# Performance work log

Hardware: AMD Instinct MI355X
Metric: run time of the kernel (lower is better)

The kernel has to match this reference:

```python
import jax, jax.numpy as jnp
import numpy as np

COMMITMENT = 0.25

def setup_inputs() -> dict:
    key = jax.random.key(0)
    k1, k2 = jax.random.split(key)
    x = jax.random.normal(k1, (64, 256, 32, 32), dtype=jnp.float32)
    embed = jax.random.normal(k2, (256, 1024), dtype=jnp.float32)  # [emb_dim, num_emb]
    return {"x": x, "embed": embed}

def reference(x, embed):
    # x: [B, C, H, W] -> NHWC
    xt = jnp.transpose(x, (0, 2, 3, 1))              # [B, H, W, C]
    B, H, W, C = xt.shape
    flat = xt.reshape(-1, C)                         # [N, C]
    # squared euclidean distances to each codebook column
    dist = (jnp.sum(flat * flat, axis=1, keepdims=True)
            - 2.0 * flat @ embed
            + jnp.sum(embed * embed, axis=0, keepdims=True))  # [N, num_emb]
    embed_idx = jnp.argmin(dist, axis=1).reshape(B, H, W)     # [B, H, W]
    quantize = embed.T[embed_idx]                    # [B, H, W, C]
    e_latent_loss = jnp.mean((jax.lax.stop_gradient(quantize) - xt) ** 2)
    q_latent_loss = jnp.mean((quantize - jax.lax.stop_gradient(xt)) ** 2)
    loss = q_latent_loss + COMMITMENT * e_latent_loss
    # straight-through estimator
    quantize = xt + jax.lax.stop_gradient(quantize - xt)
    quantize = jnp.transpose(quantize, (0, 3, 1, 2))  # back to NCHW
    return quantize, loss, embed_idx
```

## Files before the change

### kernel.cpp

```cpp
#include <hip/hip_runtime.h>

#define CDIM 256
#define HW   1024
#define NPIX 65536
#define KDIM 1024
#define TAU  0.5f
#define RB   4
#define SWZ(c) (((c) & 31) ^ (((c) >> 3) & 24))

using bf16x8 = __attribute__((ext_vector_type(8))) short;
using f32x4  = __attribute__((ext_vector_type(4))) float;
typedef unsigned int u32;

static __device__ __forceinline__ unsigned short f2bf(float v) {
    union { float f; unsigned u; } a; a.f = v;
    unsigned u = a.u;
    u += 0x7fffu + ((u >> 16) & 1u);
    return (unsigned short)(u >> 16);
}

static __device__ __forceinline__ void gload_lds16(const void* g, void* s) {
    __builtin_amdgcn_global_load_lds(
        (const __attribute__((address_space(1))) u32*)g,
        (__attribute__((address_space(3))) u32*)s,
        16, 0, 0);
}

__global__ void ee_kernel(const float* __restrict__ embed, float* __restrict__ ee) {
    int k = blockIdx.x * 256 + threadIdx.x;
    float s = 0.f;
#pragma unroll 8
    for (int c = 0; c < CDIM; ++c) {
        float v = embed[c * KDIM + k];
        s += v * v;
    }
    ee[k] = s;
}

__global__ void transpose_e(const float* __restrict__ embed, float* __restrict__ embedT) {
    __shared__ float tl[32][33];
    const int t = threadIdx.x;
    const int j = t & 31, r = t >> 5;
    const int k0 = (blockIdx.x & 31) * 32;
    const int c0 = (blockIdx.x >> 5) * 32;
#pragma unroll
    for (int rr = 0; rr < 4; ++rr) {
        int c = r * 4 + rr;
        tl[c][j] = embed[(size_t)(c0 + c) * KDIM + k0 + j];
    }
    __syncthreads();
#pragma unroll
    for (int rr = 0; rr < 4; ++rr) {
        int k = r * 4 + rr;
        embedT[(size_t)(k0 + k) * CDIM + c0 + j] = tl[j][k];
    }
}

__global__ void prep_e(const float* __restrict__ embed, short* __restrict__ e_hi) {
    int tid = blockIdx.x * 256 + threadIdx.x;
    int l  = tid & 63;
    int f  = tid >> 6;
    int nf = f & 3;
    int ks = (f >> 2) & 7;
    int nh = (f >> 5) & 1;
    int nt = f >> 6;
    int n  = nt * 128 + (nh * 4 + nf) * 16 + (l & 15);
    int c0 = ks * 32 + (l >> 4) * 8;
    bf16x8 h8;
#pragma unroll
    for (int j = 0; j < 8; ++j)
        h8[j] = (short)f2bf(-2.0f * embed[(c0 + j) * KDIM + n]);
    *(bf16x8*)&e_hi[(size_t)tid * 8] = h8;
}

__launch_bounds__(256, 2)
__global__ void vq_gemm(const float* __restrict__ x, const short* __restrict__ e_hi,
                        const float* __restrict__ ee,
                        float* __restrict__ hv1, float* __restrict__ hv2,
                        int* __restrict__ hidx) {
    __shared__ short Bs[2][8192];
    const int t  = threadIdx.x;
    const int l  = t & 63;
    const int w  = t >> 6;
    const int lr = l & 15;
    const int lg = l >> 4;
    const int tile    = blockIdx.x >> 2;
    const int quarter = blockIdx.x & 3;
    const int px0 = tile * 256 + w * 64;
    const int b   = px0 >> 10;
    const int p0  = px0 & 1023;
    const float* xb = x + (size_t)b * CDIM * HW;

    const int c_first = quarter * 8;
    {
        const int slab = w * 4;
        const char* srcb = (const char*)e_hi +
            (size_t)(((c_first >> 2) * 2 + ((c_first >> 1) & 1)) * 32 + (c_first & 1) * 2) * 1024 + l * 16;
        char* dstb = (char*)&Bs[0][0] + (size_t)slab * 1024 + l * 16;
#pragma unroll
        for (int i = 0; i < 4; ++i) {
            int s = slab + i;
            gload_lds16(srcb + (size_t)((s >> 1) * 4 + (s & 1)) * 1024, dstb + (size_t)i * 1024);
        }
    }

    bf16x8 a[4][8];
#pragma unroll
    for (int mf = 0; mf < 4; ++mf) {
#pragma unroll
        for (int ks = 0; ks < 8; ++ks) {
            const float* p = xb + (size_t)(ks * 32 + lg * 8) * HW + p0 + mf * 16 + lr;
            float v[8];
#pragma unroll
            for (int j = 0; j < 8; ++j) v[j] = p[(size_t)j * HW];
#pragma unroll
            for (int j = 0; j < 8; ++j) a[mf][ks][j] = (short)f2bf(v[j]);
        }
    }

    float minv[16], min2v[16];
    int   mini[16];
#pragma unroll
    for (int r = 0; r < 16; ++r) { minv[r] = 3.4e38f; min2v[r] = 3.4e38f; mini[r] = 0; }

    __syncthreads();

    for (int cc = 0; cc < 8; ++cc) {
        const int c   = c_first + cc;
        const int cur = cc & 1;
        if (cc < 7) {
            const int cn = c + 1;
            const int slab = w * 4;
            const char* srcb = (const char*)e_hi +
                (size_t)(((cn >> 2) * 2 + ((cn >> 1) & 1)) * 32 + (cn & 1) * 2) * 1024 + l * 16;
            char* dstb = (char*)&Bs[cur ^ 1][0] + (size_t)slab * 1024 + l * 16;
#pragma unroll
            for (int i = 0; i < 4; ++i) {
                int s = slab + i;
                gload_lds16(srcb + (size_t)((s >> 1) * 4 + (s & 1)) * 1024, dstb + (size_t)i * 1024);
            }
        }

        f32x4 acc[4][2];
#pragma unroll
        for (int mf = 0; mf < 4; ++mf)
#pragma unroll
            for (int nfi = 0; nfi < 2; ++nfi)
                acc[mf][nfi] = (f32x4){0.f, 0.f, 0.f, 0.f};

#pragma unroll
        for (int ks = 0; ks < 8; ++ks) {
#pragma unroll
            for (int nfi = 0; nfi < 2; ++nfi) {
                bf16x8 bh = *(const bf16x8*)&Bs[cur][((ks * 2 + nfi) * 64 + l) * 8];
#pragma unroll
                for (int mf = 0; mf < 4; ++mf)
                    acc[mf][nfi] = __builtin_amdgcn_mfma_f32_16x16x32_bf16(a[mf][ks], bh, acc[mf][nfi], 0, 0, 0);
            }
        }

#pragma unroll
        for (int nfi = 0; nfi < 2; ++nfi) {
            const int kg = c * 32 + nfi * 16 + lr;
            const float eev = ee[kg];
#pragma unroll
            for (int mf = 0; mf < 4; ++mf)
#pragma unroll
                for (int j = 0; j < 4; ++j) {
                    const int r = mf * 4 + j;
                    float m = acc[mf][nfi][j] + eev;
                    bool lt = m < minv[r];
                    float sec = lt ? minv[r] : m;
                    minv[r] = lt ? m : minv[r];
                    mini[r] = lt ? kg : mini[r];
                    min2v[r] = fminf(min2v[r], sec);
                }
        }
        __syncthreads();
    }

#pragma unroll
    for (int r = 0; r < 16; ++r) {
        float v1 = minv[r]; int i1 = mini[r]; float v2 = min2v[r];
#pragma unroll
        for (int mask = 1; mask < 16; mask <<= 1) {
            float ov1 = __shfl_xor(v1, mask, 64);
            int   oi1 = __shfl_xor(i1, mask, 64);
            float ov2 = __shfl_xor(v2, mask, 64);
            float vmax = fmaxf(v1, ov1);
            v2 = fminf(fminf(v2, ov2), vmax);
            bool take = (ov1 < v1) || (ov1 == v1 && oi1 < i1);
            v1 = take ? ov1 : v1;
            i1 = take ? oi1 : i1;
        }
        if (lr == 0) {
            int px = px0 + (r >> 2) * 16 + lg * 4 + (r & 3);
            int o = quarter * NPIX + px;
            hv1[o] = v1; hv2[o] = v2; hidx[o] = i1;
        }
    }
}

__global__ void merge_quarters(const float* __restrict__ hv1, const float* __restrict__ hv2,
                               const int* __restrict__ hidx, int* __restrict__ idx_out,
                               int* __restrict__ worklist, int* __restrict__ wcount) {
    int px = blockIdx.x * 256 + threadIdx.x;
    float v1 = hv1[px], v2 = hv2[px];
    int   i1 = hidx[px];
#pragma unroll
    for (int q = 1; q < 4; ++q) {
        float va = hv1[q * NPIX + px];
        float sa = hv2[q * NPIX + px];
        int   ia = hidx[q * NPIX + px];
        if (va < v1) {
            v2 = fminf(v1, sa);
            v1 = va; i1 = ia;
        } else {
            v2 = fminf(v2, va);
        }
    }
    idx_out[px] = i1;
    if (v2 - v1 < TAU) {
        int pos = atomicAdd(wcount, 1);
        worklist[pos] = px;
    }
}

__launch_bounds__(256)
__global__ void vq_rescue(const float* __restrict__ x, const float* __restrict__ embed,
                          const float* __restrict__ ee,
                          const int* __restrict__ worklist, const int* __restrict__ wcount,
                          int* __restrict__ idx_out) {
    __shared__ float xs[RB][CDIM];
    __shared__ int   pxs[RB];
    __shared__ float redv[4][RB];
    __shared__ int   redi[4][RB];
    const int t  = threadIdx.x;
    const int wv = t >> 6, ln = t & 63;
    const int cnt = *wcount;
    for (int base = blockIdx.x * RB; base < cnt; base += gridDim.x * RB) {
        const int nb = min(RB, cnt - base);
        __syncthreads();
        if (t < RB) pxs[t] = worklist[base + (t < nb ? t : nb - 1)];
        __syncthreads();
#pragma unroll
        for (int i = 0; i < RB; ++i) {
            int gn = pxs[i];
            xs[i][t] = x[(size_t)(gn >> 10) * CDIM * HW + (size_t)t * HW + (gn & 1023)];
        }
        __syncthreads();

        float4 acc[RB];
#pragma unroll
        for (int i = 0; i < RB; ++i) acc[i] = make_float4(0.f, 0.f, 0.f, 0.f);
#pragma unroll 4
        for (int c = 0; c < CDIM; ++c) {
            float4 ev = *(const float4*)&embed[c * KDIM + t * 4];
#pragma unroll
            for (int i = 0; i < RB; ++i) {
                float xv = xs[i][c];
                acc[i].x = fmaf(xv, ev.x, acc[i].x);
                acc[i].y = fmaf(xv, ev.y, acc[i].y);
                acc[i].z = fmaf(xv, ev.z, acc[i].z);
                acc[i].w = fmaf(xv, ev.w, acc[i].w);
            }
        }
        const float4 eev = *(const float4*)&ee[t * 4];
#pragma unroll
        for (int i = 0; i < RB; ++i) {
            float d0 = fmaf(-2.f, acc[i].x, eev.x);
            float d1 = fmaf(-2.f, acc[i].y, eev.y);
            float d2 = fmaf(-2.f, acc[i].z, eev.z);
            float d3 = fmaf(-2.f, acc[i].w, eev.w);
            float v = d0; int ix = t * 4;
            if (d1 < v) { v = d1; ix = t * 4 + 1; }
            if (d2 < v) { v = d2; ix = t * 4 + 2; }
            if (d3 < v) { v = d3; ix = t * 4 + 3; }
#pragma unroll
            for (int mask = 1; mask < 64; mask <<= 1) {
                float ov = __shfl_xor(v, mask, 64);
                int   oi = __shfl_xor(ix, mask, 64);
                bool take = (ov < v) || (ov == v && oi < ix);
                v = take ? ov : v; ix = take ? oi : ix;
            }
            if (ln == 0) { redv[wv][i] = v; redi[wv][i] = ix; }
        }
        __syncthreads();
        if (t < nb) {
            float fv = redv[0][t]; int fi = redi[0][t];
#pragma unroll
            for (int q = 1; q < 4; ++q) {
                float v = redv[q][t]; int ix = redi[q][t];
                if (v < fv || (v == fv && ix < fi)) { fv = v; fi = ix; }
            }
            idx_out[pxs[t]] = fi;
        }
    }
}

__launch_bounds__(256)
__global__ void vq_epilogue(const float* __restrict__ x, const float* __restrict__ embed,
                            const float* __restrict__ embedT, int useT,
                            const int* __restrict__ idx_in, float* __restrict__ out_q,
                            float* __restrict__ out_idx, float* __restrict__ partials) {
    __shared__ float q[16384];
    __shared__ int   idxs[128];
    __shared__ float lred[4];
    const int t = threadIdx.x;
    const int w = t >> 6, l = t & 63;
    const int n0 = blockIdx.x * 128;
    const int b  = n0 >> 10;

    if (t < 128) idxs[t] = idx_in[n0 + t];
    __syncthreads();
    if (t < 128) out_idx[n0 + t] = (float)idxs[t];

    const int j  = t >> 2;
    const int qd = t & 3;
    float lsum = 0.f;

#pragma unroll
    for (int pass = 0; pass < 2; ++pass) {
        const int myidx = idxs[pass * 64 + j];
        if (useT) {
            const float4* src4 = (const float4*)embedT + (size_t)myidx * 64;
#pragma unroll
            for (int i = 0; i < 16; ++i) {
                float4 v = src4[qd * 16 + i];
                int c = qd * 64 + i * 4;
                q[(c + 0) * 64 + (j ^ SWZ(c + 0))] = v.x;
                q[(c + 1) * 64 + (j ^ SWZ(c + 1))] = v.y;
                q[(c + 2) * 64 + (j ^ SWZ(c + 2))] = v.z;
                q[(c + 3) * 64 + (j ^ SWZ(c + 3))] = v.w;
            }
        } else {
#pragma unroll 4
            for (int i = 0; i < 64; ++i) {
                int c = qd * 64 + i;
                q[c * 64 + (j ^ SWZ(c))] = embed[(size_t)c * KDIM + myidx];
            }
        }
        __syncthreads();

        const int p0 = (n0 & 1023) + pass * 64;
        const size_t xbase = (size_t)b * CDIM * HW + p0;
#pragma unroll 8
        for (int ci = 0; ci < 64; ++ci) {
            int c = w * 64 + ci;
            float qv = q[c * 64 + (l ^ SWZ(c))];
            float xv = x[xbase + (size_t)c * HW + l];
            out_q[xbase + (size_t)c * HW + l] = qv;
            float d = qv - xv;
            lsum = fmaf(d, d, lsum);
        }
        __syncthreads();
    }

#pragma unroll
    for (int off = 32; off > 0; off >>= 1)
        lsum += __shfl_down(lsum, off, 64);
    if (l == 0) lred[w] = lsum;
    __syncthreads();
    if (t == 0)
        partials[blockIdx.x] = (lred[0] + lred[1]) + (lred[2] + lred[3]);
}

__global__ void loss_kernel(const float* __restrict__ partials, float* __restrict__ out_loss) {
    __shared__ float s[256];
    s[threadIdx.x] = partials[threadIdx.x] + partials[threadIdx.x + 256];
    __syncthreads();
    for (int off = 128; off > 0; off >>= 1) {
        if (threadIdx.x < off) s[threadIdx.x] += s[threadIdx.x + off];
        __syncthreads();
    }
    if (threadIdx.x == 0)
        out_loss[0] = 1.25f * s[0] / 16777216.0f;
}

extern "C" void kernel_launch(void* const* d_in, const int* in_sizes, int n_in,
                              void* d_out, int out_size, void* d_ws, size_t ws_size,
                              hipStream_t stream) {
    const float* x     = (const float*)d_in[0];
    const float* embed = (const float*)d_in[1];
    float* out_q    = (float*)d_out;
    float* out_loss = out_q + (size_t)NPIX * CDIM;
    float* out_idx  = out_loss + 1;
    int*   idx_i32  = (int*)out_idx;

    short* e_hi     = (short*)out_q;
    int*   worklist = (int*)(out_q + 131072);
    float* hv1      = out_q + 196608;
    float* hv2      = out_q + 458752;
    int*   hidx     = (int*)(out_q + 720896);

    float* ws       = (float*)d_ws;
    float* ee       = ws;
    int*   wcount   = (int*)(ws + 1024);
    float* partials = ws + 1088;
    float* embedT   = ws + 1600;
    int useT = (ws_size >= (size_t)(1600 + 262144) * sizeof(float)) ? 1 : 0;

    ee_kernel<<<KDIM / 256, 256, 0, stream>>>(embed, ee);
    if (useT) transpose_e<<<256, 256, 0, stream>>>(embed, embedT);
    prep_e<<<128, 256, 0, stream>>>(embed, e_hi);
    hipMemsetAsync(wcount, 0, 4, stream);
    vq_gemm<<<1024, 256, 0, stream>>>(x, e_hi, ee, hv1, hv2, hidx);
    merge_quarters<<<NPIX / 256, 256, 0, stream>>>(hv1, hv2, hidx, idx_i32, worklist, wcount);
    vq_rescue<<<1024, 256, 0, stream>>>(x, embed, ee, worklist, wcount, idx_i32);
    vq_epilogue<<<NPIX / 128, 256, 0, stream>>>(x, embed, useT ? embedT : embed, useT,
                                                idx_i32, out_q, out_idx, partials);
    loss_kernel<<<1, 256, 0, stream>>>(partials, out_loss);
}
```

Before: 189.9 us.

## Pack distance and index into sortable keys, halve GEMM tile for higher occupancy

The vq_gemm kernel now processes 32 pixels per wave instead of 64 and launches twice as many blocks, with launch bounds raised to 4 blocks per CU, to cut register pressure. The running min/second-min tracking is replaced by packed uint32 keys: distances are biased by +2048 so they stay positive, their low 10 mantissa bits are replaced with the codebook index, and plain integer min/max does the argmin. This drops the separate index registers and makes the shuffle reduction cheaper. The truncated distances lose precision, so the rescue threshold TAU is raised to 1.0, which may send more pixels to the exact rescue path.

```diff
diff --git a/kernel.cpp b/kernel.cpp
--- a/kernel.cpp
+++ b/kernel.cpp
@@ -4,7 +4,7 @@
 #define HW   1024
 #define NPIX 65536
 #define KDIM 1024
-#define TAU  0.5f
+#define TAU  1.0f
 #define RB   4
 #define SWZ(c) (((c) & 31) ^ (((c) >> 3) & 24))
 
@@ -26,7 +26,15 @@
         16, 0, 0);
 }
 
-__global__ void ee_kernel(const float* __restrict__ embed, float* __restrict__ ee) {
+static __device__ __forceinline__ u32 fbits(float f) {
+    union { float f; u32 u; } a; a.f = f; return a.u;
+}
+static __device__ __forceinline__ float bitsf(u32 u) {
+    union { u32 u; float f; } a; a.u = u; return a.f;
+}
+
+__global__ void ee_kernel(const float* __restrict__ embed, float* __restrict__ ee,
+                          float* __restrict__ eeb) {
     int k = blockIdx.x * 256 + threadIdx.x;
     float s = 0.f;
 #pragma unroll 8
@@ -35,6 +43,7 @@
         s += v * v;
     }
     ee[k] = s;
+    eeb[k] = s + 2048.0f;
 }
 
 __global__ void transpose_e(const float* __restrict__ embed, float* __restrict__ embedT) {
@@ -73,9 +82,9 @@
     *(bf16x8*)&e_hi[(size_t)tid * 8] = h8;
 }
 
-__launch_bounds__(256, 2)
+__launch_bounds__(256, 4)
 __global__ void vq_gemm(const float* __restrict__ x, const short* __restrict__ e_hi,
-                        const float* __restrict__ ee,
+                        const float* __restrict__ eeb,
                         float* __restrict__ hv1, float* __restrict__ hv2,
                         int* __restrict__ hidx) {
     __shared__ short Bs[2][8192];
@@ -84,9 +93,9 @@
     const int w  = t >> 6;
     const int lr = l & 15;
     const int lg = l >> 4;
-    const int tile    = blockIdx.x >> 2;
-    const int quarter = blockIdx.x & 3;
-    const int px0 = tile * 256 + w * 64;
+    const int tile    = blockIdx.x & 511;
+    const int quarter = blockIdx.x >> 9;
+    const int px0 = tile * 128 + w * 32;
     const int b   = px0 >> 10;
     const int p0  = px0 & 1023;
     const float* xb = x + (size_t)b * CDIM * HW;
@@ -104,9 +113,9 @@
         }
     }
 
-    bf16x8 a[4][8];
-#pragma unroll
-    for (int mf = 0; mf < 4; ++mf) {
+    bf16x8 a[2][8];
+#pragma unroll
+    for (int mf = 0; mf < 2; ++mf) {
 #pragma unroll
         for (int ks = 0; ks < 8; ++ks) {
             const float* p = xb + (size_t)(ks * 32 + lg * 8) * HW + p0 + mf * 16 + lr;
@@ -118,10 +127,9 @@
         }
     }
 
-    float minv[16], min2v[16];
-    int   mini[16];
-#pragma unroll
-    for (int r = 0; r < 16; ++r) { minv[r] = 3.4e38f; min2v[r] = 3.4e38f; mini[r] = 0; }
+    u32 min1k[8], min2k[8];
+#pragma unroll
+    for (int r = 0; r < 8; ++r) { min1k[r] = 0xFFFFFFFFu; min2k[r] = 0xFFFFFFFFu; }
 
     __syncthreads();
 
@@ -141,9 +149,9 @@
             }
         }
 
-        f32x4 acc[4][2];
-#pragma unroll
-        for (int mf = 0; mf < 4; ++mf)
+        f32x4 acc[2][2];
+#pragma unroll
+        for (int mf = 0; mf < 2; ++mf)
 #pragma unroll
             for (int nfi = 0; nfi < 2; ++nfi)
                 acc[mf][nfi] = (f32x4){0.f, 0.f, 0.f, 0.f};
@@ -154,7 +162,7 @@
             for (int nfi = 0; nfi < 2; ++nfi) {
                 bf16x8 bh = *(const bf16x8*)&Bs[cur][((ks * 2 + nfi) * 64 + l) * 8];
 #pragma unroll
-                for (int mf = 0; mf < 4; ++mf)
+                for (int mf = 0; mf < 2; ++mf)
                     acc[mf][nfi] = __builtin_amdgcn_mfma_f32_16x16x32_bf16(a[mf][ks], bh, acc[mf][nfi], 0, 0, 0);
             }
         }
@@ -162,41 +170,36 @@
 #pragma unroll
         for (int nfi = 0; nfi < 2; ++nfi) {
             const int kg = c * 32 + nfi * 16 + lr;
-            const float eev = ee[kg];
-#pragma unroll
-            for (int mf = 0; mf < 4; ++mf)
+            const float ebv = eeb[kg];
+#pragma unroll
+            for (int mf = 0; mf < 2; ++mf)
 #pragma unroll
                 for (int j = 0; j < 4; ++j) {
                     const int r = mf * 4 + j;
-                    float m = acc[mf][nfi][j] + eev;
-                    bool lt = m < minv[r];
-                    float sec = lt ? minv[r] : m;
-                    minv[r] = lt ? m : minv[r];
-                    mini[r] = lt ? kg : mini[r];
-                    min2v[r] = fminf(min2v[r], sec);
+                    u32 key = (fbits(acc[mf][nfi][j] + ebv) & 0xFFFFFC00u) | (u32)kg;
+                    min2k[r] = min(min2k[r], max(key, min1k[r]));
+                    min1k[r] = min(min1k[r], key);
                 }
         }
         __syncthreads();
     }
 
 #pragma unroll
-    for (int r = 0; r < 16; ++r) {
-        float v1 = minv[r]; int i1 = mini[r]; float v2 = min2v[r];
+    for (int r = 0; r < 8; ++r) {
+        u32 k1 = min1k[r], k2 = min2k[r];
 #pragma unroll
         for (int mask = 1; mask < 16; mask <<= 1) {
-            float ov1 = __shfl_xor(v1, mask, 64);
-            int   oi1 = __shfl_xor(i1, mask, 64);
-            float ov2 = __shfl_xor(v2, mask, 64);
-            float vmax = fmaxf(v1, ov1);
-            v2 = fminf(fminf(v2, ov2), vmax);
-            bool take = (ov1 < v1) || (ov1 == v1 && oi1 < i1);
-            v1 = take ? ov1 : v1;
-            i1 = take ? oi1 : i1;
+            u32 ok1 = (u32)__shfl_xor((int)k1, mask, 64);
+            u32 ok2 = (u32)__shfl_xor((int)k2, mask, 64);
+            k2 = min(min(k2, ok2), max(k1, ok1));
+            k1 = min(k1, ok1);
         }
         if (lr == 0) {
             int px = px0 + (r >> 2) * 16 + lg * 4 + (r & 3);
             int o = quarter * NPIX + px;
-            hv1[o] = v1; hv2[o] = v2; hidx[o] = i1;
+            hv1[o] = bitsf(k1 & 0xFFFFFC00u);
+            hv2[o] = bitsf(k2 & 0xFFFFFC00u);
+            hidx[o] = (int)(k1 & 1023u);
         }
     }
 }
@@ -395,16 +398,17 @@
 
     float* ws       = (float*)d_ws;
     float* ee       = ws;
-    int*   wcount   = (int*)(ws + 1024);
-    float* partials = ws + 1088;
-    float* embedT   = ws + 1600;
-    int useT = (ws_size >= (size_t)(1600 + 262144) * sizeof(float)) ? 1 : 0;
-
-    ee_kernel<<<KDIM / 256, 256, 0, stream>>>(embed, ee);
+    float* eeb      = ws + 1024;
+    int*   wcount   = (int*)(ws + 2048);
+    float* partials = ws + 2112;
+    float* embedT   = ws + 2624;
+    int useT = (ws_size >= (size_t)(2624 + 262144) * sizeof(float)) ? 1 : 0;
+
+    ee_kernel<<<KDIM / 256, 256, 0, stream>>>(embed, ee, eeb);
     if (useT) transpose_e<<<256, 256, 0, stream>>>(embed, embedT);
     prep_e<<<128, 256, 0, stream>>>(embed, e_hi);
     hipMemsetAsync(wcount, 0, 4, stream);
-    vq_gemm<<<1024, 256, 0, stream>>>(x, e_hi, ee, hv1, hv2, hidx);
+    vq_gemm<<<2048, 256, 0, stream>>>(x, e_hi, eeb, hv1, hv2, hidx);
     merge_quarters<<<NPIX / 256, 256, 0, stream>>>(hv1, hv2, hidx, idx_i32, worklist, wcount);
     vq_rescue<<<1024, 256, 0, stream>>>(x, embed, ee, worklist, wcount, idx_i32);
     vq_epilogue<<<NPIX / 128, 256, 0, stream>>>(x, embed, useT ? embedT : embed, useT,
```

Result: slower. 205.4 us (+8.1%).
